# Kernel tuning notes

Measured on AMD Instinct MI355X. Metric: run time of the kernel, lower is better.

## Reference

```python
import jax, jax.numpy as jnp
import numpy as np

EPS = 1e-6

def _rms(x, g):
    # RMSNorm over last dim (head_dim)
    return x * jax.lax.rsqrt(jnp.mean(x * x, axis=-1, keepdims=True) + EPS) * g

def _split_heads(x, h):
    b, l, hd = x.shape
    return x.reshape(b, l, h, hd // h).transpose(0, 2, 1, 3)  # b h l d

def setup_inputs() -> dict:
    key = jax.random.key(0)
    ks = jax.random.split(key, 10)
    B, Limg, Lip, D, Dip, Temb = 1, 2048, 512, 3072, 1280, 1280
    return {
        "ip_hidden_states": jax.random.normal(ks[0], (B, Lip, Dip), jnp.float32),
        "img_query": jax.random.normal(ks[1], (B, Limg, D), jnp.float32),
        "img_key": jax.random.normal(ks[2], (B, Limg, D), jnp.float32),
        "img_value": jax.random.normal(ks[3], (B, Limg, D), jnp.float32),
        "t_emb": jax.random.normal(ks[4], (B, Temb), jnp.float32),
        "w_ada": jax.random.normal(ks[5], (2 * Dip, Temb), jnp.float32) * 0.02,
        "b_ada": jnp.zeros((2 * Dip,), jnp.float32),
        "w_k_ip": jax.random.normal(ks[6], (D, Dip), jnp.float32) * 0.02,
        "w_v_ip": jax.random.normal(ks[7], (D, Dip), jnp.float32) * 0.02,
        "g_q": jnp.ones((128,), jnp.float32),
        "g_k": jnp.ones((128,), jnp.float32),
        "g_ipk": jnp.ones((128,), jnp.float32),
        "n_heads": 24,
    }

def reference(ip_hidden_states, img_query, img_key, img_value, t_emb,
              w_ada, b_ada, w_k_ip, w_v_ip, g_q, g_k, g_ipk, n_heads):
    # AdaLayerNorm ('normal' mode): silu + linear -> shift/scale, LayerNorm (no affine)
    e = jax.nn.silu(t_emb) @ w_ada.T + b_ada              # [B, 2*Dip]
    shift, scale = jnp.split(e, 2, axis=1)
    mu = jnp.mean(ip_hidden_states, axis=-1, keepdims=True)
    var = jnp.var(ip_hidden_states, axis=-1, keepdims=True)
    xn = (ip_hidden_states - mu) * jax.lax.rsqrt(var + EPS)
    ip_norm = xn * (1.0 + scale[:, None]) + shift[:, None]  # [B, Lip, Dip]

    ip_key = ip_norm @ w_k_ip.T                            # [B, Lip, D]
    ip_value = ip_norm @ w_v_ip.T

    q = _split_heads(img_query, n_heads)                   # [B, H, Limg, d]
    k = _split_heads(img_key, n_heads)
    v = _split_heads(img_value, n_heads)
    ipk = _split_heads(ip_key, n_heads)                    # [B, H, Lip, d]
    ipv = _split_heads(ip_value, n_heads)

    q = _rms(q, g_q)
    k = _rms(k, g_k)
    ipk = _rms(ipk, g_ipk)

    key_all = jnp.concatenate([k, ipk], axis=2)            # [B, H, Limg+Lip, d]
    val_all = jnp.concatenate([v, ipv], axis=2)

    d = q.shape[-1]
    scores = jnp.einsum('bhqd,bhkd->bhqk', q, key_all) * (1.0 / np.sqrt(d))
    probs = jax.nn.softmax(scores, axis=-1)
    out = jnp.einsum('bhqk,bhkd->bhqd', probs, val_all)    # [B, H, Limg, d]

    b, h, l, dd = out.shape
    return out.transpose(0, 2, 1, 3).reshape(b, l, h * dd)
```

## Files before the change

kernel.cpp:

```cpp
#include <hip/hip_runtime.h>
#include <math.h>

#define H    24
#define Dh   128
#define LIMG 2048
#define LIP  512
#define DM   3072
#define DIP  1280
#define LK   2560
#define EPSF 1e-6f
#define SM_SCALE 0.08838834764831845f
#define C2EXP 0.12751930f
#define THRU 90.50967f

#define EXP2F(x) __builtin_exp2f(x)

typedef __attribute__((ext_vector_type(8))) short bf16x8;
typedef __attribute__((ext_vector_type(4))) float f32x4;

typedef const unsigned int __attribute__((address_space(1))) gu32;
typedef unsigned int __attribute__((address_space(3))) lu32;

static __device__ __forceinline__ unsigned short f2bf(float x) {
  union { float f; unsigned u; } v; v.f = x;
  unsigned r = v.u + 0x7fffu + ((v.u >> 16) & 1u);
  return (unsigned short)(r >> 16);
}

static __device__ __forceinline__ float bf2f(unsigned short b) {
  union { unsigned u; float f; } v; v.u = ((unsigned)b) << 16;
  return v.f;
}

__global__ __launch_bounds__(256) void ada_kernel(
    const float* __restrict__ t_emb, const float* __restrict__ w_ada,
    const float* __restrict__ b_ada, float* __restrict__ e) {
  int j = blockIdx.x;
  int tid = threadIdx.x;
  const float* wrow = w_ada + (long)j * DIP;
  float acc = 0.f;
  for (int k = tid; k < DIP; k += 256) {
    float t = t_emb[k];
    acc += (t / (1.f + expf(-t))) * wrow[k];
  }
#pragma unroll
  for (int m = 1; m < 64; m <<= 1) acc += __shfl_xor(acc, m, 64);
  __shared__ float red[4];
  if ((tid & 63) == 0) red[tid >> 6] = acc;
  __syncthreads();
  if (tid == 0) e[j] = red[0] + red[1] + red[2] + red[3] + b_ada[j];
}

__global__ __launch_bounds__(256) void adaln_kernel(
    const float* __restrict__ x, const float* __restrict__ e,
    unsigned short* __restrict__ ipnh, unsigned short* __restrict__ ipnl) {
  int r = blockIdx.x;
  int tid = threadIdx.x;
  const float* xr = x + (long)r * DIP;
  float v[5];
  float s = 0.f, ss = 0.f;
#pragma unroll
  for (int i = 0; i < 5; i++) {
    v[i] = xr[tid + i * 256];
    s += v[i];
    ss += v[i] * v[i];
  }
#pragma unroll
  for (int m = 1; m < 64; m <<= 1) {
    s += __shfl_xor(s, m, 64);
    ss += __shfl_xor(ss, m, 64);
  }
  __shared__ float rs_[4], rss_[4];
  if ((tid & 63) == 0) { rs_[tid >> 6] = s; rss_[tid >> 6] = ss; }
  __syncthreads();
  s = rs_[0] + rs_[1] + rs_[2] + rs_[3];
  ss = rss_[0] + rss_[1] + rss_[2] + rss_[3];
  float mu = s * (1.f / DIP);
  float var = ss * (1.f / DIP) - mu * mu;
  float rstd = rsqrtf(var + EPSF);
  unsigned short* oh = ipnh + (long)r * DIP;
  unsigned short* ol = ipnl + (long)r * DIP;
#pragma unroll
  for (int i = 0; i < 5; i++) {
    int c = tid + i * 256;
    float o = (v[i] - mu) * rstd * (1.f + e[DIP + c]) + e[c];
    unsigned short hb = f2bf(o);
    oh[c] = hb;
    ol[c] = f2bf(o - bf2f(hb));
  }
}

__global__ __launch_bounds__(256) void prep_kernel(
    const float* __restrict__ k_in, const float* __restrict__ v_in,
    const float* __restrict__ g_k,
    unsigned short* __restrict__ Kb, unsigned short* __restrict__ Vt) {
  __shared__ unsigned short Vls[128][33];
  int h = blockIdx.y, l0 = blockIdx.x * 32;
  int tid = threadIdx.x;
  int r = tid >> 3, c = tid & 7;
  const float* ksrc = k_in + (long)(l0 + r) * DM + h * Dh + c * 16;
  const float* vsrc = v_in + (long)(l0 + r) * DM + h * Dh + c * 16;
  float kv[16], vv[16];
  float ssq = 0.f;
#pragma unroll
  for (int i = 0; i < 4; i++) {
    float4 a = *(const float4*)(ksrc + i * 4);
    float4 b = *(const float4*)(vsrc + i * 4);
    kv[i*4+0]=a.x; kv[i*4+1]=a.y; kv[i*4+2]=a.z; kv[i*4+3]=a.w;
    vv[i*4+0]=b.x; vv[i*4+1]=b.y; vv[i*4+2]=b.z; vv[i*4+3]=b.w;
    ssq += a.x*a.x + a.y*a.y + a.z*a.z + a.w*a.w;
  }
  ssq += __shfl_xor(ssq, 1, 8);
  ssq += __shfl_xor(ssq, 2, 8);
  ssq += __shfl_xor(ssq, 4, 8);
  float rstd = rsqrtf(ssq * (1.f / Dh) + EPSF);
  unsigned short kb[16];
#pragma unroll
  for (int i = 0; i < 16; i++) kb[i] = f2bf(kv[i] * rstd * g_k[c * 16 + i]);
  unsigned short* kdst = Kb + ((long)h * LK + l0 + r) * Dh + c * 16;
  *(uint4*)(kdst) = *(uint4*)(kb);
  *(uint4*)(kdst + 8) = *(uint4*)(kb + 8);
#pragma unroll
  for (int i = 0; i < 16; i++) Vls[c * 16 + i][r] = f2bf(vv[i]);
  __syncthreads();
  if (tid < 128) {
    int d = tid;
    unsigned short ov[32];
#pragma unroll
    for (int j = 0; j < 32; j++) ov[j] = Vls[d][j];
    unsigned short* vdst = Vt + ((long)h * Dh + d) * LK + l0;
    *(uint4*)(vdst)      = *(uint4*)(ov);
    *(uint4*)(vdst + 8)  = *(uint4*)(ov + 8);
    *(uint4*)(vdst + 16) = *(uint4*)(ov + 16);
    *(uint4*)(vdst + 24) = *(uint4*)(ov + 24);
  }
}

__global__ __launch_bounds__(256) void proj_kernel(
    const unsigned short* __restrict__ Ah, const unsigned short* __restrict__ Al,
    const float* __restrict__ Wk, const float* __restrict__ Wv,
    const float* __restrict__ g_ipk,
    unsigned short* __restrict__ Kb, unsigned short* __restrict__ Vt) {
  __shared__ __align__(16) unsigned short lds_u[24576];
  const float* W = blockIdx.z ? Wv : Wk;
  int h = blockIdx.y;
  int m0 = blockIdx.x * 64;
  int tid = threadIdx.x;
  int w = tid >> 6, lane = tid & 63;
  int m = lane & 15, quad = lane >> 4;

  const float* wrow = W + (long)(h * Dh + (tid & 127)) * DIP + ((tid >> 7) << 3);
  const unsigned short* garow_h = Ah + (long)(m0 + lane) * DIP + w * 8;
  const unsigned short* garow_l = Al + (long)(m0 + lane) * DIP + w * 8;

  f32x4 acc[8];
#pragma unroll
  for (int i = 0; i < 8; i++) acc[i] = (f32x4){0.f, 0.f, 0.f, 0.f};

  float4 wa = *(const float4*)(wrow);
  float4 wb = *(const float4*)(wrow + 4);
  float4 wc = *(const float4*)(wrow + 16);
  float4 wd = *(const float4*)(wrow + 20);

  auto stagek = [&](int b, int k0) {
    float cur[16] = {wa.x, wa.y, wa.z, wa.w, wb.x, wb.y, wb.z, wb.w,
                     wc.x, wc.y, wc.z, wc.w, wd.x, wd.y, wd.z, wd.w};
    if (k0 + 32 < DIP) {
      wa = *(const float4*)(wrow + k0 + 32);
      wb = *(const float4*)(wrow + k0 + 36);
      wc = *(const float4*)(wrow + k0 + 48);
      wd = *(const float4*)(wrow + k0 + 52);
    }
    unsigned short hi[16], lo[16];
#pragma unroll
    for (int i = 0; i < 16; i++) {
      unsigned short hb = f2bf(cur[i]);
      hi[i] = hb;
      lo[i] = f2bf(cur[i] - bf2f(hb));
    }
    unsigned short* AhsB = lds_u + b * 12288;
    unsigned short* AlsB = AhsB + 2048;
    unsigned short* WhsB = AhsB + 4096;
    unsigned short* WlsB = AhsB + 8192;
    __builtin_amdgcn_global_load_lds((gu32*)(garow_h + k0), (lu32*)(AhsB + w * 512), 16, 0, 0);
    __builtin_amdgcn_global_load_lds((gu32*)(garow_l + k0), (lu32*)(AlsB + w * 512), 16, 0, 0);
    *(uint4*)(WhsB + tid * 8) = *(uint4*)(hi);
    *(uint4*)(WlsB + tid * 8) = *(uint4*)(lo);
    *(uint4*)(WhsB + (tid + 256) * 8) = *(uint4*)(hi + 8);
    *(uint4*)(WlsB + (tid + 256) * 8) = *(uint4*)(lo + 8);
  };

  stagek(0, 0);
  __syncthreads();
  int buf = 0;
#pragma unroll 1
  for (int k0 = 0; k0 < DIP; k0 += 32) {
    if (k0 + 32 < DIP) stagek(buf ^ 1, k0 + 32);
    unsigned short* AhsB = lds_u + buf * 12288;
    unsigned short* AlsB = AhsB + 2048;
    unsigned short* WhsB = AhsB + 4096;
    unsigned short* WlsB = AhsB + 8192;
    bf16x8 ahf = *(const bf16x8*)(AhsB + ((quad << 6) + (w << 4) + m) * 8);
    bf16x8 alf = *(const bf16x8*)(AlsB + ((quad << 6) + (w << 4) + m) * 8);
#pragma unroll
    for (int nt = 0; nt < 8; nt++) {
      bf16x8 bhf = *(const bf16x8*)(WhsB + ((quad << 7) + (nt << 4) + m) * 8);
      bf16x8 blf = *(const bf16x8*)(WlsB + ((quad << 7) + (nt << 4) + m) * 8);
      acc[nt] = __builtin_amdgcn_mfma_f32_16x16x32_bf16(ahf, bhf, acc[nt], 0, 0, 0);
      acc[nt] = __builtin_amdgcn_mfma_f32_16x16x32_bf16(ahf, blf, acc[nt], 0, 0, 0);
      acc[nt] = __builtin_amdgcn_mfma_f32_16x16x32_bf16(alf, bhf, acc[nt], 0, 0, 0);
    }
    __syncthreads();
    buf ^= 1;
  }

  if (blockIdx.z == 0) {
    float gkv[8];
#pragma unroll
    for (int nt = 0; nt < 8; nt++) gkv[nt] = g_ipk[nt * 16 + m];
#pragma unroll
    for (int r = 0; r < 4; r++) {
      float ssq = 0.f;
#pragma unroll
      for (int nt = 0; nt < 8; nt++) ssq += acc[nt][r] * acc[nt][r];
      ssq += __shfl_xor(ssq, 1, 16);
      ssq += __shfl_xor(ssq, 2, 16);
      ssq += __shfl_xor(ssq, 4, 16);
      ssq += __shfl_xor(ssq, 8, 16);
      float rstd = rsqrtf(ssq * (1.f / Dh) + EPSF);
      long row = (long)h * LK + LIMG + m0 + w * 16 + quad * 4 + r;
#pragma unroll
      for (int nt = 0; nt < 8; nt++)
        Kb[row * Dh + nt * 16 + m] = f2bf(acc[nt][r] * rstd * gkv[nt]);
    }
  } else {
#pragma unroll
    for (int nt = 0; nt < 8; nt++) {
      ushort4 o;
      o.x = f2bf(acc[nt][0]); o.y = f2bf(acc[nt][1]);
      o.z = f2bf(acc[nt][2]); o.w = f2bf(acc[nt][3]);
      *(ushort4*)(Vt + ((long)h * Dh + nt * 16 + m) * LK + LIMG + m0 + w * 16 + quad * 4) = o;
    }
  }
}

__global__ __launch_bounds__(256, 4) void flash_kernel(
    const float* __restrict__ q_in, const float* __restrict__ g_q,
    const unsigned short* __restrict__ Kb, const unsigned short* __restrict__ Vt,
    float* __restrict__ out) {
  __shared__ __align__(16) unsigned char lds[16384 + 16384 + 5120];
  unsigned short* Ks = (unsigned short*)lds;
  unsigned short* Vs = (unsigned short*)(lds + 16384);
  unsigned short* Ps = (unsigned short*)(lds + 32768);
  int tid = threadIdx.x;
  int w = tid >> 6, lid = tid & 63;
  int m = lid & 15, quad = lid >> 4;
  int id = blockIdx.x;
  int sidx = id >> 3;
  int h = (id & 7) * 3 + (sidx >> 5);
  int q0 = (sidx & 31) * 64;
  int qrow = q0 + w * 16 + m;

  bf16x8 aq[4];
  {
    float qf[4][8];
    float ssq = 0.f;
    const float* qsrc = q_in + (long)qrow * DM + h * Dh + quad * 8;
#pragma unroll
    for (int ks = 0; ks < 4; ks++) {
      float4 a = *(const float4*)(qsrc + ks * 32);
      float4 b = *(const float4*)(qsrc + ks * 32 + 4);
      qf[ks][0]=a.x; qf[ks][1]=a.y; qf[ks][2]=a.z; qf[ks][3]=a.w;
      qf[ks][4]=b.x; qf[ks][5]=b.y; qf[ks][6]=b.z; qf[ks][7]=b.w;
      ssq += a.x*a.x + a.y*a.y + a.z*a.z + a.w*a.w;
      ssq += b.x*b.x + b.y*b.y + b.z*b.z + b.w*b.w;
    }
    ssq += __shfl_xor(ssq, 16, 64);
    ssq += __shfl_xor(ssq, 32, 64);
    float rstd = rsqrtf(ssq * (1.f / Dh) + EPSF);
    const float* gq = g_q + quad * 8;
#pragma unroll
    for (int ks = 0; ks < 4; ks++) {
      float4 ga = *(const float4*)(gq + ks * 32);
      float4 gb = *(const float4*)(gq + ks * 32 + 4);
      float gg[8] = {ga.x, ga.y, ga.z, ga.w, gb.x, gb.y, gb.z, gb.w};
#pragma unroll
      for (int j = 0; j < 8; j++)
        aq[ks][j] = (short)f2bf(qf[ks][j] * rstd * gg[j]);
    }
  }

  const unsigned short* KbH = Kb + (long)h * LK * Dh;
  const unsigned short* VtH = Vt + (long)h * Dh * LK;
  unsigned short* Pw = Ps + w * 640;

  f32x4 acc_o[8];
#pragma unroll
  for (int i = 0; i < 8; i++) acc_o[i] = (f32x4){0.f, 0.f, 0.f, 0.f};
  float mrun = -INFINITY;
  float lrun = 0.f;

  auto stage = [&](int b, int j0) {
    unsigned short* KsB = Ks + b * 4096;
    unsigned short* VsB = Vs + b * 4096;
    int sbase = w * 128;
#pragma unroll
    for (int is = 0; is < 2; is++) {
      int s = sbase + is * 64 + lid;
      int r = s >> 4, cc = s & 15;
      int c = cc ^ (r & 15);
      const unsigned short* g = KbH + (long)(j0 + r) * Dh + c * 8;
      __builtin_amdgcn_global_load_lds((gu32*)g, (lu32*)(KsB + (sbase + is * 64) * 8),
                                       16, 0, 0);
    }
#pragma unroll
    for (int is = 0; is < 2; is++) {
      int s = sbase + is * 64 + lid;
      int d = s >> 2, cc = s & 3;
      int c = cc ^ (d & 3);
      const unsigned short* g = VtH + (long)d * LK + j0 + c * 8;
      __builtin_amdgcn_global_load_lds((gu32*)g, (lu32*)(VsB + (sbase + is * 64) * 8),
                                       16, 0, 0);
    }
  };

  stage(0, 0);
  __syncthreads();
  int buf = 0;
#pragma unroll 1
  for (int jt = 0; jt < LK / 32; ++jt) {
    if (jt + 1 < LK / 32) stage(buf ^ 1, (jt + 1) * 32);
    unsigned short* KsB = Ks + buf * 4096;
    unsigned short* VsB = Vs + buf * 4096;

    f32x4 sc[2];
    sc[0] = (f32x4){0.f, 0.f, 0.f, 0.f};
    sc[1] = (f32x4){0.f, 0.f, 0.f, 0.f};
    __builtin_amdgcn_s_setprio(1);
#pragma unroll
    for (int t = 0; t < 2; t++)
#pragma unroll
      for (int ks = 0; ks < 4; ks++) {
        int rr = t * 16 + m;
        int g = (ks * 4 + quad) ^ m;
        bf16x8 bk = *(const bf16x8*)(KsB + rr * 128 + g * 8);
        sc[t] = __builtin_amdgcn_mfma_f32_16x16x32_bf16(bk, aq[ks], sc[t], 0, 0, 0);
      }
    __builtin_amdgcn_s_setprio(0);

    float pv[8] = {sc[0][0], sc[0][1], sc[0][2], sc[0][3],
                   sc[1][0], sc[1][1], sc[1][2], sc[1][3]};
    float t0 = fmaxf(fmaxf(pv[0], pv[1]), fmaxf(pv[2], pv[3]));
    float t1 = fmaxf(fmaxf(pv[4], pv[5]), fmaxf(pv[6], pv[7]));
    float tmax = fmaxf(t0, t1);
    tmax = fmaxf(tmax, __shfl_xor(tmax, 16, 64));
    tmax = fmaxf(tmax, __shfl_xor(tmax, 32, 64));
    int noresc = __all(tmax <= mrun + THRU);
    float al = 1.f;
    if (!noresc) {
      float mnew = fmaxf(mrun, tmax);
      al = EXP2F((mrun - mnew) * C2EXP);
      mrun = mnew;
    }
    float p[8];
    unsigned short pb[8];
#pragma unroll
    for (int j = 0; j < 8; j++) {
      p[j] = EXP2F((pv[j] - mrun) * C2EXP);
      pb[j] = f2bf(p[j]);
    }
    float rsum = (p[0] + p[1]) + (p[2] + p[3]) + (p[4] + p[5]) + (p[6] + p[7]);
    rsum += __shfl_xor(rsum, 16, 64);
    rsum += __shfl_xor(rsum, 32, 64);
    lrun = lrun * al + rsum;

    uint2 pk0, pk1;
    pk0.x = (unsigned)pb[0] | ((unsigned)pb[1] << 16);
    pk0.y = (unsigned)pb[2] | ((unsigned)pb[3] << 16);
    pk1.x = (unsigned)pb[4] | ((unsigned)pb[5] << 16);
    pk1.y = (unsigned)pb[6] | ((unsigned)pb[7] << 16);
    *(uint2*)(Pw + m * 40 + quad * 4) = pk0;
    *(uint2*)(Pw + m * 40 + 16 + quad * 4) = pk1;
    __threadfence_block();
    bf16x8 ap = *(const bf16x8*)(Pw + m * 40 + quad * 8);

    if (!noresc) {
      float alr[4];
#pragma unroll
      for (int r = 0; r < 4; r++) alr[r] = __shfl(al, quad * 4 + r, 16);
#pragma unroll
      for (int dt = 0; dt < 8; dt++) {
        acc_o[dt][0] *= alr[0]; acc_o[dt][1] *= alr[1];
        acc_o[dt][2] *= alr[2]; acc_o[dt][3] *= alr[3];
      }
    }

    __builtin_amdgcn_s_setprio(1);
#pragma unroll
    for (int dt = 0; dt < 8; dt++) {
      bf16x8 bv = *(const bf16x8*)(VsB + ((dt * 16 + m) * 4 + (quad ^ (m & 3))) * 8);
      acc_o[dt] = __builtin_amdgcn_mfma_f32_16x16x32_bf16(ap, bv, acc_o[dt], 0, 0, 0);
    }
    __builtin_amdgcn_s_setprio(0);
    __syncthreads();
    buf ^= 1;
  }

  float inv = 1.f / lrun;
  float ilr[4];
#pragma unroll
  for (int r = 0; r < 4; r++) ilr[r] = __shfl(inv, quad * 4 + r, 16);
#pragma unroll
  for (int dt = 0; dt < 8; dt++)
#pragma unroll
    for (int r = 0; r < 4; r++)
      out[(long)(q0 + w * 16 + quad * 4 + r) * DM + h * Dh + dt * 16 + m] =
          acc_o[dt][r] * ilr[r];
}

extern "C" void kernel_launch(void* const* d_in, const int* in_sizes, int n_in,
                              void* d_out, int out_size, void* d_ws, size_t ws_size,
                              hipStream_t stream) {
  const float* ip_hidden = (const float*)d_in[0];
  const float* img_q     = (const float*)d_in[1];
  const float* img_k     = (const float*)d_in[2];
  const float* img_v     = (const float*)d_in[3];
  const float* t_emb     = (const float*)d_in[4];
  const float* w_ada     = (const float*)d_in[5];
  const float* b_ada     = (const float*)d_in[6];
  const float* w_k_ip    = (const float*)d_in[7];
  const float* w_v_ip    = (const float*)d_in[8];
  const float* g_q       = (const float*)d_in[9];
  const float* g_k       = (const float*)d_in[10];
  const float* g_ipk     = (const float*)d_in[11];

  char* base = (char*)d_ws;
  float* e = (float*)base;
  unsigned short* ipnh = (unsigned short*)(base + 16384);
  unsigned short* ipnl = (unsigned short*)(base + 1327104);
  unsigned short* Kb   = (unsigned short*)(base + 2637824);
  unsigned short* Vt   = Kb + (size_t)H * LK * Dh;
  float* out = (float*)d_out;

  ada_kernel<<<2 * DIP, 256, 0, stream>>>(t_emb, w_ada, b_ada, e);
  adaln_kernel<<<LIP, 256, 0, stream>>>(ip_hidden, e, ipnh, ipnl);
  prep_kernel<<<dim3(LIMG / 32, H), 256, 0, stream>>>(img_k, img_v, g_k, Kb, Vt);
  proj_kernel<<<dim3(LIP / 64, H, 2), 256, 0, stream>>>(ipnh, ipnl, w_k_ip, w_v_ip,
                                                        g_ipk, Kb, Vt);
  flash_kernel<<<dim3(768), 256, 0, stream>>>(img_q, g_q, Kb, Vt, out);
}
```

Measured before the change: 393.1 us.

## Process two query tiles per wave and tile V transposed into contiguous chunks

Each flash-attention wave now handles 32 query rows (two 16-row groups), so every K and V tile loaded into LDS is reused for twice as many MFMAs. The grid is halved to 384 blocks and launch bounds drop to 3 blocks per CU. Separately, the transposed V buffer is stored as contiguous 32-key chunks of 4096 elements, so each stage load becomes a pointer increment with a new swizzle. The trade-off is higher register pressure and fewer blocks, leaving only 384 blocks on a large GPU, which may underfill the CUs.

```diff
diff --git a/kernel.cpp b/kernel.cpp
--- a/kernel.cpp
+++ b/kernel.cpp
@@ -128,7 +128,7 @@
     unsigned short ov[32];
 #pragma unroll
     for (int j = 0; j < 32; j++) ov[j] = Vls[d][j];
-    unsigned short* vdst = Vt + ((long)h * Dh + d) * LK + l0;
+    unsigned short* vdst = Vt + ((long)h * 80 + (l0 >> 5)) * 4096 + d * 32;
     *(uint4*)(vdst)      = *(uint4*)(ov);
     *(uint4*)(vdst + 8)  = *(uint4*)(ov + 8);
     *(uint4*)(vdst + 16) = *(uint4*)(ov + 16);
@@ -234,21 +234,23 @@
         Kb[row * Dh + nt * 16 + m] = f2bf(acc[nt][r] * rstd * gkv[nt]);
     }
   } else {
+    int l0q = LIMG + m0 + w * 16 + quad * 4;
+    unsigned short* vbase = Vt + ((long)h * 80 + (l0q >> 5)) * 4096 + (l0q & 31);
 #pragma unroll
     for (int nt = 0; nt < 8; nt++) {
       ushort4 o;
       o.x = f2bf(acc[nt][0]); o.y = f2bf(acc[nt][1]);
       o.z = f2bf(acc[nt][2]); o.w = f2bf(acc[nt][3]);
-      *(ushort4*)(Vt + ((long)h * Dh + nt * 16 + m) * LK + LIMG + m0 + w * 16 + quad * 4) = o;
-    }
-  }
-}
-
-__global__ __launch_bounds__(256, 4) void flash_kernel(
+      *(ushort4*)(vbase + (nt * 16 + m) * 32) = o;
+    }
+  }
+}
+
+__global__ __launch_bounds__(256, 3) void flash_kernel(
     const float* __restrict__ q_in, const float* __restrict__ g_q,
     const unsigned short* __restrict__ Kb, const unsigned short* __restrict__ Vt,
     float* __restrict__ out) {
-  __shared__ __align__(16) unsigned char lds[16384 + 16384 + 5120];
+  __shared__ __align__(16) unsigned char lds[16384 + 16384 + 10240];
   unsigned short* Ks = (unsigned short*)lds;
   unsigned short* Vs = (unsigned short*)(lds + 16384);
   unsigned short* Ps = (unsigned short*)(lds + 32768);
@@ -257,14 +259,15 @@
   int m = lid & 15, quad = lid >> 4;
   int id = blockIdx.x;
   int sidx = id >> 3;
-  int h = (id & 7) * 3 + (sidx >> 5);
-  int q0 = (sidx & 31) * 64;
-  int qrow = q0 + w * 16 + m;
-
-  bf16x8 aq[4];
-  {
+  int h = (id & 7) * 3 + (sidx >> 4);
+  int q0 = (sidx & 15) * 128;
+
+  bf16x8 aq[2][4];
+#pragma unroll
+  for (int g2 = 0; g2 < 2; g2++) {
     float qf[4][8];
     float ssq = 0.f;
+    int qrow = q0 + w * 32 + g2 * 16 + m;
     const float* qsrc = q_in + (long)qrow * DM + h * Dh + quad * 8;
 #pragma unroll
     for (int ks = 0; ks < 4; ks++) {
@@ -286,56 +289,57 @@
       float gg[8] = {ga.x, ga.y, ga.z, ga.w, gb.x, gb.y, gb.z, gb.w};
 #pragma unroll
       for (int j = 0; j < 8; j++)
-        aq[ks][j] = (short)f2bf(qf[ks][j] * rstd * gg[j]);
+        aq[g2][ks][j] = (short)f2bf(qf[ks][j] * rstd * gg[j]);
     }
   }
 
   const unsigned short* KbH = Kb + (long)h * LK * Dh;
-  const unsigned short* VtH = Vt + (long)h * Dh * LK;
-  unsigned short* Pw = Ps + w * 640;
-
-  f32x4 acc_o[8];
-#pragma unroll
-  for (int i = 0; i < 8; i++) acc_o[i] = (f32x4){0.f, 0.f, 0.f, 0.f};
-  float mrun = -INFINITY;
-  float lrun = 0.f;
-
-  auto stage = [&](int b, int j0) {
+  const unsigned short* VtH = Vt + (long)h * 80 * 4096;
+  unsigned short* Pw0 = Ps + (w * 2 + 0) * 640;
+  unsigned short* Pw1 = Ps + (w * 2 + 1) * 640;
+
+  int s0 = w * 128 + lid, s1 = s0 + 64;
+  int rK0 = s0 >> 4, cK0 = (s0 & 15) ^ (rK0 & 15);
+  int rK1 = s1 >> 4, cK1 = (s1 & 15) ^ (rK1 & 15);
+  const unsigned short* pK0 = KbH + (long)rK0 * Dh + cK0 * 8;
+  const unsigned short* pK1 = KbH + (long)rK1 * Dh + cK1 * 8;
+  int dV0 = s0 >> 2, cV0 = (s0 & 3) ^ ((dV0 >> 1) & 3);
+  int dV1 = s1 >> 2, cV1 = (s1 & 3) ^ ((dV1 >> 1) & 3);
+  const unsigned short* pV0 = VtH + dV0 * 32 + cV0 * 8;
+  const unsigned short* pV1 = VtH + dV1 * 32 + cV1 * 8;
+
+  f32x4 acc0[8], acc1[8];
+#pragma unroll
+  for (int i = 0; i < 8; i++) {
+    acc0[i] = (f32x4){0.f, 0.f, 0.f, 0.f};
+    acc1[i] = (f32x4){0.f, 0.f, 0.f, 0.f};
+  }
+  float mrun0 = -INFINITY, mrun1 = -INFINITY;
+  float lrun0 = 0.f, lrun1 = 0.f;
+
+  auto stage = [&](int b) {
     unsigned short* KsB = Ks + b * 4096;
     unsigned short* VsB = Vs + b * 4096;
-    int sbase = w * 128;
-#pragma unroll
-    for (int is = 0; is < 2; is++) {
-      int s = sbase + is * 64 + lid;
-      int r = s >> 4, cc = s & 15;
-      int c = cc ^ (r & 15);
-      const unsigned short* g = KbH + (long)(j0 + r) * Dh + c * 8;
-      __builtin_amdgcn_global_load_lds((gu32*)g, (lu32*)(KsB + (sbase + is * 64) * 8),
-                                       16, 0, 0);
-    }
-#pragma unroll
-    for (int is = 0; is < 2; is++) {
-      int s = sbase + is * 64 + lid;
-      int d = s >> 2, cc = s & 3;
-      int c = cc ^ (d & 3);
-      const unsigned short* g = VtH + (long)d * LK + j0 + c * 8;
-      __builtin_amdgcn_global_load_lds((gu32*)g, (lu32*)(VsB + (sbase + is * 64) * 8),
-                                       16, 0, 0);
-    }
+    __builtin_amdgcn_global_load_lds((gu32*)pK0, (lu32*)(KsB + (w * 128) * 8), 16, 0, 0);
+    __builtin_amdgcn_global_load_lds((gu32*)pK1, (lu32*)(KsB + (w * 128 + 64) * 8), 16, 0, 0);
+    __builtin_amdgcn_global_load_lds((gu32*)pV0, (lu32*)(VsB + (w * 128) * 8), 16, 0, 0);
+    __builtin_amdgcn_global_load_lds((gu32*)pV1, (lu32*)(VsB + (w * 128 + 64) * 8), 16, 0, 0);
+    pK0 += 4096; pK1 += 4096;
+    pV0 += 4096; pV1 += 4096;
   };
 
-  stage(0, 0);
+  stage(0);
   __syncthreads();
   int buf = 0;
 #pragma unroll 1
   for (int jt = 0; jt < LK / 32; ++jt) {
-    if (jt + 1 < LK / 32) stage(buf ^ 1, (jt + 1) * 32);
+    if (jt + 1 < LK / 32) stage(buf ^ 1);
     unsigned short* KsB = Ks + buf * 4096;
     unsigned short* VsB = Vs + buf * 4096;
 
-    f32x4 sc[2];
-    sc[0] = (f32x4){0.f, 0.f, 0.f, 0.f};
-    sc[1] = (f32x4){0.f, 0.f, 0.f, 0.f};
+    f32x4 sc0[2], sc1[2];
+    sc0[0] = (f32x4){0.f,0.f,0.f,0.f}; sc0[1] = (f32x4){0.f,0.f,0.f,0.f};
+    sc1[0] = (f32x4){0.f,0.f,0.f,0.f}; sc1[1] = (f32x4){0.f,0.f,0.f,0.f};
     __builtin_amdgcn_s_setprio(1);
 #pragma unroll
     for (int t = 0; t < 2; t++)
@@ -344,78 +348,135 @@
         int rr = t * 16 + m;
         int g = (ks * 4 + quad) ^ m;
         bf16x8 bk = *(const bf16x8*)(KsB + rr * 128 + g * 8);
-        sc[t] = __builtin_amdgcn_mfma_f32_16x16x32_bf16(bk, aq[ks], sc[t], 0, 0, 0);
+        sc0[t] = __builtin_amdgcn_mfma_f32_16x16x32_bf16(bk, aq[0][ks], sc0[t], 0, 0, 0);
+        sc1[t] = __builtin_amdgcn_mfma_f32_16x16x32_bf16(bk, aq[1][ks], sc1[t], 0, 0, 0);
       }
     __builtin_amdgcn_s_setprio(0);
 
-    float pv[8] = {sc[0][0], sc[0][1], sc[0][2], sc[0][3],
-                   sc[1][0], sc[1][1], sc[1][2], sc[1][3]};
-    float t0 = fmaxf(fmaxf(pv[0], pv[1]), fmaxf(pv[2], pv[3]));
-    float t1 = fmaxf(fmaxf(pv[4], pv[5]), fmaxf(pv[6], pv[7]));
-    float tmax = fmaxf(t0, t1);
-    tmax = fmaxf(tmax, __shfl_xor(tmax, 16, 64));
-    tmax = fmaxf(tmax, __shfl_xor(tmax, 32, 64));
-    int noresc = __all(tmax <= mrun + THRU);
-    float al = 1.f;
-    if (!noresc) {
-      float mnew = fmaxf(mrun, tmax);
-      al = EXP2F((mrun - mnew) * C2EXP);
-      mrun = mnew;
-    }
-    float p[8];
-    unsigned short pb[8];
-#pragma unroll
-    for (int j = 0; j < 8; j++) {
-      p[j] = EXP2F((pv[j] - mrun) * C2EXP);
-      pb[j] = f2bf(p[j]);
-    }
-    float rsum = (p[0] + p[1]) + (p[2] + p[3]) + (p[4] + p[5]) + (p[6] + p[7]);
-    rsum += __shfl_xor(rsum, 16, 64);
-    rsum += __shfl_xor(rsum, 32, 64);
-    lrun = lrun * al + rsum;
-
-    uint2 pk0, pk1;
-    pk0.x = (unsigned)pb[0] | ((unsigned)pb[1] << 16);
-    pk0.y = (unsigned)pb[2] | ((unsigned)pb[3] << 16);
-    pk1.x = (unsigned)pb[4] | ((unsigned)pb[5] << 16);
-    pk1.y = (unsigned)pb[6] | ((unsigned)pb[7] << 16);
-    *(uint2*)(Pw + m * 40 + quad * 4) = pk0;
-    *(uint2*)(Pw + m * 40 + 16 + quad * 4) = pk1;
-    __threadfence_block();
-    bf16x8 ap = *(const bf16x8*)(Pw + m * 40 + quad * 8);
-
-    if (!noresc) {
+    float al0 = 1.f, al1 = 1.f;
+    int nr0, nr1;
+    {
+      float pv[8] = {sc0[0][0], sc0[0][1], sc0[0][2], sc0[0][3],
+                     sc0[1][0], sc0[1][1], sc0[1][2], sc0[1][3]};
+      float tmax = fmaxf(fmaxf(fmaxf(pv[0],pv[1]), fmaxf(pv[2],pv[3])),
+                         fmaxf(fmaxf(pv[4],pv[5]), fmaxf(pv[6],pv[7])));
+      tmax = fmaxf(tmax, __shfl_xor(tmax, 16, 64));
+      tmax = fmaxf(tmax, __shfl_xor(tmax, 32, 64));
+      nr0 = __all(tmax <= mrun0 + THRU);
+      if (!nr0) {
+        float mn = fmaxf(mrun0, tmax);
+        al0 = EXP2F((mrun0 - mn) * C2EXP);
+        mrun0 = mn;
+      }
+      float p[8]; unsigned short pb[8];
+#pragma unroll
+      for (int j = 0; j < 8; j++) {
+        p[j] = EXP2F((pv[j] - mrun0) * C2EXP);
+        pb[j] = f2bf(p[j]);
+      }
+      float rs = (p[0]+p[1]) + (p[2]+p[3]) + (p[4]+p[5]) + (p[6]+p[7]);
+      rs += __shfl_xor(rs, 16, 64);
+      rs += __shfl_xor(rs, 32, 64);
+      lrun0 = lrun0 * al0 + rs;
+      uint2 pk0, pk1;
+      pk0.x = (unsigned)pb[0] | ((unsigned)pb[1] << 16);
+      pk0.y = (unsigned)pb[2] | ((unsigned)pb[3] << 16);
+      pk1.x = (unsigned)pb[4] | ((unsigned)pb[5] << 16);
+      pk1.y = (unsigned)pb[6] | ((unsigned)pb[7] << 16);
+      *(uint2*)(Pw0 + m * 40 + quad * 4) = pk0;
+      *(uint2*)(Pw0 + m * 40 + 16 + quad * 4) = pk1;
+    }
+    {
+      float pv[8] = {sc1[0][0], sc1[0][1], sc1[0][2], sc1[0][3],
+                     sc1[1][0], sc1[1][1], sc1[1][2], sc1[1][3]};
+      float tmax = fmaxf(fmaxf(fmaxf(pv[0],pv[1]), fmaxf(pv[2],pv[3])),
+                         fmaxf(fmaxf(pv[4],pv[5]), fmaxf(pv[6],pv[7])));
+      tmax = fmaxf(tmax, __shfl_xor(tmax, 16, 64));
+      tmax = fmaxf(tmax, __shfl_xor(tmax, 32, 64));
+      nr1 = __all(tmax <= mrun1 + THRU);
+      if (!nr1) {
+        float mn = fmaxf(mrun1, tmax);
+        al1 = EXP2F((mrun1 - mn) * C2EXP);
+        mrun1 = mn;
+      }
+      float p[8]; unsigned short pb[8];
+#pragma unroll
+      for (int j = 0; j < 8; j++) {
+        p[j] = EXP2F((pv[j] - mrun1) * C2EXP);
+        pb[j] = f2bf(p[j]);
+      }
+      float rs = (p[0]+p[1]) + (p[2]+p[3]) + (p[4]+p[5]) + (p[6]+p[7]);
+      rs += __shfl_xor(rs, 16, 64);
+      rs += __shfl_xor(rs, 32, 64);
+      lrun1 = lrun1 * al1 + rs;
+      uint2 pk0, pk1;
+      pk0.x = (unsigned)pb[0] | ((unsigned)pb[1] << 16);
+      pk0.y = (unsigned)pb[2] | ((unsigned)pb[3] << 16);
+      pk1.x = (unsigned)pb[4] | ((unsigned)pb[5] << 16);
+      pk1.y = (unsigned)pb[6] | ((unsigned)pb[7] << 16);
+      *(uint2*)(Pw1 + m * 40 + quad * 4) = pk0;
+      *(uint2*)(Pw1 + m * 40 + 16 + quad * 4) = pk1;
+    }
+    bf16x8 ap0 = *(const bf16x8*)(Pw0 + m * 40 + quad * 8);
+    bf16x8 ap1 = *(const bf16x8*)(Pw1 + m * 40 + quad * 8);
+
+    if (!nr0) {
       float alr[4];
 #pragma unroll
-      for (int r = 0; r < 4; r++) alr[r] = __shfl(al, quad * 4 + r, 16);
+      for (int r = 0; r < 4; r++) alr[r] = __shfl(al0, quad * 4 + r, 16);
 #pragma unroll
       for (int dt = 0; dt < 8; dt++) {
-        acc_o[dt][0] *= alr[0]; acc_o[dt][1] *= alr[1];
-        acc_o[dt][2] *= alr[2]; acc_o[dt][3] *= alr[3];
+        acc0[dt][0] *= alr[0]; acc0[dt][1] *= alr[1];
+        acc0[dt][2] *= alr[2]; acc0[dt][3] *= alr[3];
+      }
+    }
+    if (!nr1) {
+      float alr[4];
+#pragma unroll
+      for (int r = 0; r < 4; r++) alr[r] = __shfl(al1, quad * 4 + r, 16);
+#pragma unroll
+      for (int dt = 0; dt < 8; dt++) {
+        acc1[dt][0] *= alr[0]; acc1[dt][1] *= alr[1];
+        acc1[dt][2] *= alr[2]; acc1[dt][3] *= alr[3];
       }
     }
 
     __builtin_amdgcn_s_setprio(1);
 #pragma unroll
     for (int dt = 0; dt < 8; dt++) {
-      bf16x8 bv = *(const bf16x8*)(VsB + ((dt * 16 + m) * 4 + (quad ^ (m & 3))) * 8);
-      acc_o[dt] = __builtin_amdgcn_mfma_f32_16x16x32_bf16(ap, bv, acc_o[dt], 0, 0, 0);
+      bf16x8 bv = *(const bf16x8*)(VsB + ((dt * 16 + m) * 4 + (quad ^ ((m >> 1) & 3))) * 8);
+      acc0[dt] = __builtin_amdgcn_mfma_f32_16x16x32_bf16(ap0, bv, acc0[dt], 0, 0, 0);
+      acc1[dt] = __builtin_amdgcn_mfma_f32_16x16x32_bf16(ap1, bv, acc1[dt], 0, 0, 0);
     }
     __builtin_amdgcn_s_setprio(0);
     __syncthreads();
     buf ^= 1;
   }
 
-  float inv = 1.f / lrun;
-  float ilr[4];
-#pragma unroll
-  for (int r = 0; r < 4; r++) ilr[r] = __shfl(inv, quad * 4 + r, 16);
-#pragma unroll
-  for (int dt = 0; dt < 8; dt++)
-#pragma unroll
-    for (int r = 0; r < 4; r++)
-      out[(long)(q0 + w * 16 + quad * 4 + r) * DM + h * Dh + dt * 16 + m] =
-          acc_o[dt][r] * ilr[r];
+  {
+    float inv = 1.f / lrun0;
+    float ilr[4];
+#pragma unroll
+    for (int r = 0; r < 4; r++) ilr[r] = __shfl(inv, quad * 4 + r, 16);
+#pragma unroll
+    for (int dt = 0; dt < 8; dt++)
+#pragma unroll
+      for (int r = 0; r < 4; r++)
+        out[(long)(q0 + w * 32 + quad * 4 + r) * DM + h * Dh + dt * 16 + m] =
+            acc0[dt][r] * ilr[r];
+  }
+  {
+    float inv = 1.f / lrun1;
+    float ilr[4];
+#pragma unroll
+    for (int r = 0; r < 4; r++) ilr[r] = __shfl(inv, quad * 4 + r, 16);
+#pragma unroll
+    for (int dt = 0; dt < 8; dt++)
+#pragma unroll
+      for (int r = 0; r < 4; r++)
+        out[(long)(q0 + w * 32 + 16 + quad * 4 + r) * DM + h * Dh + dt * 16 + m] =
+            acc1[dt][r] * ilr[r];
+  }
 }
 
 extern "C" void kernel_launch(void* const* d_in, const int* in_sizes, int n_in,
@@ -447,5 +508,5 @@
   prep_kernel<<<dim3(LIMG / 32, H), 256, 0, stream>>>(img_k, img_v, g_k, Kb, Vt);
   proj_kernel<<<dim3(LIP / 64, H, 2), 256, 0, stream>>>(ipnh, ipnl, w_k_ip, w_v_ip,
                                                         g_ipk, Kb, Vt);
-  flash_kernel<<<dim3(768), 256, 0, stream>>>(img_q, g_q, Kb, Vt, out);
-}
+  flash_kernel<<<dim3(384), 256, 0, stream>>>(img_q, g_q, Kb, Vt, out);
+}
```

New measurement: 419.2 us. 1.07x slower.

## Tile V^T layout into contiguous 32-key blocks and unroll flash double buffer

Applied to the files above, without the earlier changes.

V^T is now stored as per-head blocks of 32 keys x 128 dims, each laid out contiguously (4096 elements), so every staging load reads one contiguous 8KB chunk instead of strided rows. Staging pointers are precomputed once and advanced by a constant, the double-buffer loop is unrolled by two to drop buffer-index arithmetic, and the LDS swizzle for V is changed to match the new row pitch. It also removes the __threadfence_block between the P store and reload, which relies on wave-local LDS ordering for correctness.

```diff
diff --git a/kernel.cpp b/kernel.cpp
--- a/kernel.cpp
+++ b/kernel.cpp
@@ -128,7 +128,7 @@
     unsigned short ov[32];
 #pragma unroll
     for (int j = 0; j < 32; j++) ov[j] = Vls[d][j];
-    unsigned short* vdst = Vt + ((long)h * Dh + d) * LK + l0;
+    unsigned short* vdst = Vt + ((long)h * 80 + (l0 >> 5)) * 4096 + d * 32;
     *(uint4*)(vdst)      = *(uint4*)(ov);
     *(uint4*)(vdst + 8)  = *(uint4*)(ov + 8);
     *(uint4*)(vdst + 16) = *(uint4*)(ov + 16);
@@ -234,12 +234,14 @@
         Kb[row * Dh + nt * 16 + m] = f2bf(acc[nt][r] * rstd * gkv[nt]);
     }
   } else {
+    int l0q = LIMG + m0 + w * 16 + quad * 4;
+    unsigned short* vbase = Vt + ((long)h * 80 + (l0q >> 5)) * 4096 + (l0q & 31);
 #pragma unroll
     for (int nt = 0; nt < 8; nt++) {
       ushort4 o;
       o.x = f2bf(acc[nt][0]); o.y = f2bf(acc[nt][1]);
       o.z = f2bf(acc[nt][2]); o.w = f2bf(acc[nt][3]);
-      *(ushort4*)(Vt + ((long)h * Dh + nt * 16 + m) * LK + LIMG + m0 + w * 16 + quad * 4) = o;
+      *(ushort4*)(vbase + (nt * 16 + m) * 32) = o;
     }
   }
 }
@@ -291,7 +293,7 @@
   }
 
   const unsigned short* KbH = Kb + (long)h * LK * Dh;
-  const unsigned short* VtH = Vt + (long)h * Dh * LK;
+  const unsigned short* VtH = Vt + (long)h * 80 * 4096;
   unsigned short* Pw = Ps + w * 640;
 
   f32x4 acc_o[8];
@@ -300,39 +302,28 @@
   float mrun = -INFINITY;
   float lrun = 0.f;
 
-  auto stage = [&](int b, int j0) {
+  int s0 = w * 128 + lid, s1 = s0 + 64;
+  int rK0 = s0 >> 4, cK0 = (s0 & 15) ^ (rK0 & 15);
+  int rK1 = s1 >> 4, cK1 = (s1 & 15) ^ (rK1 & 15);
+  const unsigned short* pK0 = KbH + (long)rK0 * Dh + cK0 * 8;
+  const unsigned short* pK1 = KbH + (long)rK1 * Dh + cK1 * 8;
+  int dV0 = s0 >> 2, cV0 = (s0 & 3) ^ ((dV0 >> 1) & 3);
+  int dV1 = s1 >> 2, cV1 = (s1 & 3) ^ ((dV1 >> 1) & 3);
+  const unsigned short* pV0 = VtH + dV0 * 32 + cV0 * 8;
+  const unsigned short* pV1 = VtH + dV1 * 32 + cV1 * 8;
+
+  auto stage = [&](int b) {
     unsigned short* KsB = Ks + b * 4096;
     unsigned short* VsB = Vs + b * 4096;
-    int sbase = w * 128;
-#pragma unroll
-    for (int is = 0; is < 2; is++) {
-      int s = sbase + is * 64 + lid;
-      int r = s >> 4, cc = s & 15;
-      int c = cc ^ (r & 15);
-      const unsigned short* g = KbH + (long)(j0 + r) * Dh + c * 8;
-      __builtin_amdgcn_global_load_lds((gu32*)g, (lu32*)(KsB + (sbase + is * 64) * 8),
-                                       16, 0, 0);
-    }
-#pragma unroll
-    for (int is = 0; is < 2; is++) {
-      int s = sbase + is * 64 + lid;
-      int d = s >> 2, cc = s & 3;
-      int c = cc ^ (d & 3);
-      const unsigned short* g = VtH + (long)d * LK + j0 + c * 8;
-      __builtin_amdgcn_global_load_lds((gu32*)g, (lu32*)(VsB + (sbase + is * 64) * 8),
-                                       16, 0, 0);
-    }
+    __builtin_amdgcn_global_load_lds((gu32*)pK0, (lu32*)(KsB + (w * 128) * 8), 16, 0, 0);
+    __builtin_amdgcn_global_load_lds((gu32*)pK1, (lu32*)(KsB + (w * 128 + 64) * 8), 16, 0, 0);
+    __builtin_amdgcn_global_load_lds((gu32*)pV0, (lu32*)(VsB + (w * 128) * 8), 16, 0, 0);
+    __builtin_amdgcn_global_load_lds((gu32*)pV1, (lu32*)(VsB + (w * 128 + 64) * 8), 16, 0, 0);
+    pK0 += 4096; pK1 += 4096;
+    pV0 += 4096; pV1 += 4096;
   };
 
-  stage(0, 0);
-  __syncthreads();
-  int buf = 0;
-#pragma unroll 1
-  for (int jt = 0; jt < LK / 32; ++jt) {
-    if (jt + 1 < LK / 32) stage(buf ^ 1, (jt + 1) * 32);
-    unsigned short* KsB = Ks + buf * 4096;
-    unsigned short* VsB = Vs + buf * 4096;
-
+  auto compute = [&](const unsigned short* KsB, const unsigned short* VsB) {
     f32x4 sc[2];
     sc[0] = (f32x4){0.f, 0.f, 0.f, 0.f};
     sc[1] = (f32x4){0.f, 0.f, 0.f, 0.f};
@@ -381,7 +372,6 @@
     pk1.y = (unsigned)pb[6] | ((unsigned)pb[7] << 16);
     *(uint2*)(Pw + m * 40 + quad * 4) = pk0;
     *(uint2*)(Pw + m * 40 + 16 + quad * 4) = pk1;
-    __threadfence_block();
     bf16x8 ap = *(const bf16x8*)(Pw + m * 40 + quad * 8);
 
     if (!noresc) {
@@ -398,12 +388,22 @@
     __builtin_amdgcn_s_setprio(1);
 #pragma unroll
     for (int dt = 0; dt < 8; dt++) {
-      bf16x8 bv = *(const bf16x8*)(VsB + ((dt * 16 + m) * 4 + (quad ^ (m & 3))) * 8);
+      bf16x8 bv = *(const bf16x8*)(VsB + ((dt * 16 + m) * 4 + (quad ^ ((m >> 1) & 3))) * 8);
       acc_o[dt] = __builtin_amdgcn_mfma_f32_16x16x32_bf16(ap, bv, acc_o[dt], 0, 0, 0);
     }
     __builtin_amdgcn_s_setprio(0);
+  };
+
+  stage(0);
+  __syncthreads();
+#pragma unroll 1
+  for (int jt = 0; jt < LK / 32; jt += 2) {
+    stage(1);
+    compute(Ks, Vs);
     __syncthreads();
-    buf ^= 1;
+    if (jt + 2 < LK / 32) stage(0);
+    compute(Ks + 4096, Vs + 4096);
+    __syncthreads();
   }
 
   float inv = 1.f / lrun;
```

Result: faster. 384.5 us (-2.2%).
